# Kernel optimization log

Measured on AMD Instinct MI355X. Metric: run time of the kernel, lower is better.

## Reference

```python
import jax, jax.numpy as jnp
import numpy as np

B, D, H, W = 16, 128, 64, 64
K = 512  # num_embeddings


def setup_inputs() -> dict:
    key = jax.random.key(0)
    k1, k2 = jax.random.split(key)
    inputs = jax.random.normal(k1, (B, D, H, W), dtype=jnp.float32)
    embedding_weight = jax.random.normal(k2, (K, D), dtype=jnp.float32)
    return {"inputs": inputs, "embedding_weight": embedding_weight}


def reference(inputs, embedding_weight):
    # NCHW -> NHWC, flatten to [N, D]
    x = jnp.transpose(inputs, (0, 2, 3, 1))  # [B, H, W, D]
    flat = x.reshape(-1, x.shape[-1])        # [N, D]
    dists = (
        jnp.sum(flat ** 2, axis=1, keepdims=True)
        + jnp.sum(embedding_weight ** 2, axis=1)
        - 2.0 * flat @ embedding_weight.T
    )  # [N, K]
    idx = jnp.argmin(dists, axis=1)          # [N]
    # one-hot @ codebook == gather
    quantized = embedding_weight[idx].reshape(x.shape)  # [B, H, W, D]
    # straight-through estimator
    quantized = x + jax.lax.stop_gradient(quantized - x)
    return jnp.transpose(quantized, (0, 3, 1, 2))  # back to NCHW
```

## Files before the change

### kernel.cpp

```cpp
#include <hip/hip_runtime.h>


typedef _Float16 f16;
typedef _Float16 f16x4 __attribute__((ext_vector_type(4)));
typedef _Float16 f16x8 __attribute__((ext_vector_type(8)));
typedef float f32x16 __attribute__((ext_vector_type(16)));

#define ND 128
#define NK 512
#define NHW 4096
#define LO_SCALE 2048.0f
#define LO_INV (1.0f / 2048.0f)

#define WS_XHI 0
#define WS_XLO 16777216u
#define WS_EHI 33554432u
#define WS_ELO 33685504u
#define WS_ENS 33816576u
#define WS_NEED 33818624u

__global__ __launch_bounds__(256) void vq_prep(const float* __restrict__ x,
                                               const float* __restrict__ e,
                                               f16* __restrict__ xhi, f16* __restrict__ xlo,
                                               f16* __restrict__ ehi, f16* __restrict__ elo,
                                               float* __restrict__ ens) {
  const int tid = threadIdx.x;
  if (blockIdx.x < 1024) {
    __shared__ float sc[ND][65];
    const int tok0 = blockIdx.x * 64;
    const int b = blockIdx.x >> 6;
    const int hw0 = (blockIdx.x & 63) * 64;
    const float* xb = x + (size_t)b * ND * NHW + hw0;
    #pragma unroll
    for (int it = 0; it < 8; ++it) {
      const int f = tid + 256 * it;
      const int d = f >> 4, t4 = (f & 15) * 4;
      const float4 v = *(const float4*)(xb + (size_t)d * NHW + t4);
      sc[d][t4 + 0] = v.x; sc[d][t4 + 1] = v.y;
      sc[d][t4 + 2] = v.z; sc[d][t4 + 3] = v.w;
    }
    __syncthreads();
    const int oct = tid & 15, trow = tid >> 4;
    #pragma unroll
    for (int p = 0; p < 4; ++p) {
      const int t = p * 16 + trow;
      const int tok = tok0 + t;
      float v[8];
      #pragma unroll
      for (int j = 0; j < 8; ++j) v[j] = sc[oct * 8 + j][t];
      f16x8 h, l;
      #pragma unroll
      for (int j = 0; j < 8; ++j) {
        const f16 hv = (f16)v[j];
        h[j] = hv;
        l[j] = (f16)((v[j] - (float)hv) * LO_SCALE);
      }
      const size_t off = (size_t)(tok >> 5) * 4096 + oct * 256 + (tok & 31) * 8;
      *(f16x8*)(xhi + off) = h;
      *(f16x8*)(xlo + off) = l;
    }
  } else {
    const int k0 = ((int)blockIdx.x - 1024) * 16;
    const int r = tid >> 4, dq16 = tid & 15;
    const int k = k0 + r;
    float ssum = 0.0f;
    #pragma unroll
    for (int hh = 0; hh < 2; ++hh) {
      const int dq = dq16 + 16 * hh;
      const float4 v = *(const float4*)(e + (size_t)k * ND + 4 * dq);
      ssum += v.x * v.x + v.y * v.y + v.z * v.z + v.w * v.w;
      float va[4] = {v.x, v.y, v.z, v.w};
      f16x4 hv, lv;
      #pragma unroll
      for (int j = 0; j < 4; ++j) {
        const f16 h = (f16)va[j];
        hv[j] = h;
        lv[j] = (f16)((va[j] - (float)h) * LO_SCALE);
      }
      const int sl = (dq >> 1) ^ (k & 15);
      const size_t off = (size_t)k * ND + sl * 8 + (dq & 1) * 4;
      *(f16x4*)(ehi + off) = hv;
      *(f16x4*)(elo + off) = lv;
    }
    #pragma unroll
    for (int m = 1; m < 16; m <<= 1) ssum += __shfl_xor(ssum, m, 64);
    if (dq16 == 0) ens[k] = 0.5f * ssum;
  }
}

__global__ __launch_bounds__(256) void vq_score(const f16* __restrict__ xhi,
                                                const f16* __restrict__ xlo,
                                                const f16* __restrict__ ehi,
                                                const f16* __restrict__ elo,
                                                const float* __restrict__ ens,
                                                const float* __restrict__ e32,
                                                float* __restrict__ out) {
  __shared__ f16 eh_s[2][64 * 128];
  __shared__ f16 el_s[2][64 * 128];
  __shared__ float ens_s[NK];

  const int tid = threadIdx.x;
  const int w = tid >> 6;
  const int lane = tid & 63;
  const int l31 = lane & 31;
  const int half = lane >> 5;
  const int T0 = (int)blockIdx.x * 128;
  const int tok = T0 + w * 32 + l31;

  __builtin_amdgcn_global_load_lds(ehi + tid * 8,        &eh_s[0][tid * 8],        16, 0, 0);
  __builtin_amdgcn_global_load_lds(ehi + 2048 + tid * 8, &eh_s[0][2048 + tid * 8], 16, 0, 0);
  __builtin_amdgcn_global_load_lds(ehi + 4096 + tid * 8, &eh_s[0][4096 + tid * 8], 16, 0, 0);
  __builtin_amdgcn_global_load_lds(ehi + 6144 + tid * 8, &eh_s[0][6144 + tid * 8], 16, 0, 0);
  __builtin_amdgcn_global_load_lds(elo + tid * 8,        &el_s[0][tid * 8],        16, 0, 0);
  __builtin_amdgcn_global_load_lds(elo + 2048 + tid * 8, &el_s[0][2048 + tid * 8], 16, 0, 0);
  __builtin_amdgcn_global_load_lds(elo + 4096 + tid * 8, &el_s[0][4096 + tid * 8], 16, 0, 0);
  __builtin_amdgcn_global_load_lds(elo + 6144 + tid * 8, &el_s[0][6144 + tid * 8], 16, 0, 0);

  f16x8 Bh[8], Bl[8];
  {
    const size_t base = (size_t)(tok >> 5) * 4096 + (size_t)l31 * 8 + half * 256;
    #pragma unroll
    for (int ks = 0; ks < 8; ++ks) {
      Bh[ks] = *(const f16x8*)(xhi + base + ks * 512);
      Bl[ks] = *(const f16x8*)(xlo + base + ks * 512);
    }
  }
  ens_s[tid] = ens[tid];
  ens_s[tid + 256] = ens[tid + 256];
  __syncthreads();

  float bv = -3.0e38f;
  int bi = 0;
  int cur = 0;
  const int sbase = l31 & 15;

  for (int c = 0; c < 8; ++c) {
    if (c < 7) {
      const f16* gh = ehi + (c + 1) * 8192;
      const f16* gl = elo + (c + 1) * 8192;
      f16* dh = &eh_s[cur ^ 1][0];
      f16* dl = &el_s[cur ^ 1][0];
      __builtin_amdgcn_global_load_lds(gh + tid * 8,        dh + tid * 8,        16, 0, 0);
      __builtin_amdgcn_global_load_lds(gh + 2048 + tid * 8, dh + 2048 + tid * 8, 16, 0, 0);
      __builtin_amdgcn_global_load_lds(gh + 4096 + tid * 8, dh + 4096 + tid * 8, 16, 0, 0);
      __builtin_amdgcn_global_load_lds(gh + 6144 + tid * 8, dh + 6144 + tid * 8, 16, 0, 0);
      __builtin_amdgcn_global_load_lds(gl + tid * 8,        dl + tid * 8,        16, 0, 0);
      __builtin_amdgcn_global_load_lds(gl + 2048 + tid * 8, dl + 2048 + tid * 8, 16, 0, 0);
      __builtin_amdgcn_global_load_lds(gl + 4096 + tid * 8, dl + 4096 + tid * 8, 16, 0, 0);
      __builtin_amdgcn_global_load_lds(gl + 6144 + tid * 8, dl + 6144 + tid * 8, 16, 0, 0);
    }

    #pragma unroll
    for (int cg = 0; cg < 2; ++cg) {
      const int r = cg * 32 + l31;
      const f16* ah = &eh_s[cur][r * 128];
      const f16* al = &el_s[cur][r * 128];
      f32x16 a1 = {}, a2 = {};
      #pragma unroll
      for (int ks = 0; ks < 8; ++ks) {
        const int sl = ((2 * ks + half) ^ sbase) * 8;
        const f16x8 Ah = *(const f16x8*)(ah + sl);
        const f16x8 Al = *(const f16x8*)(al + sl);
        a2 = __builtin_amdgcn_mfma_f32_32x32x16_f16(Al, Bh[ks], a2, 0, 0, 0);
        a1 = __builtin_amdgcn_mfma_f32_32x32x16_f16(Ah, Bh[ks], a1, 0, 0, 0);
        a2 = __builtin_amdgcn_mfma_f32_32x32x16_f16(Ah, Bl[ks], a2, 0, 0, 0);
      }
      const int kb = c * 64 + cg * 32 + 4 * half;
      const float4 b0 = *(const float4*)&ens_s[kb + 0];
      const float4 b1 = *(const float4*)&ens_s[kb + 8];
      const float4 b2 = *(const float4*)&ens_s[kb + 16];
      const float4 b3 = *(const float4*)&ens_s[kb + 24];
      const float bias[16] = {b0.x, b0.y, b0.z, b0.w, b1.x, b1.y, b1.z, b1.w,
                              b2.x, b2.y, b2.z, b2.w, b3.x, b3.y, b3.z, b3.w};
      #pragma unroll
      for (int rr = 0; rr < 16; ++rr) {
        const float s = a1[rr] + a2[rr] * LO_INV - bias[rr];
        const int code = kb + (rr & 3) + 8 * (rr >> 2);
        if (s > bv) { bv = s; bi = code; }
      }
    }
    __syncthreads();
    cur ^= 1;
  }

  {
    const float ov = __shfl_xor(bv, 32, 64);
    const int oi = __shfl_xor(bi, 32, 64);
    if (ov > bv || (ov == bv && oi < bi)) { bv = ov; bi = oi; }
  }

  {
    const int bb = tok >> 12;
    const int hw = tok & 4095;
    const float* er = e32 + (size_t)bi * ND + half * 64;
    float* ob = out + (size_t)bb * ND * NHW + (size_t)(half * 64) * NHW + hw;
    #pragma unroll
    for (int j4 = 0; j4 < 16; ++j4) {
      const float4 ev = *(const float4*)(er + j4 * 4);
      ob[(size_t)(j4 * 4 + 0) * NHW] = ev.x;
      ob[(size_t)(j4 * 4 + 1) * NHW] = ev.y;
      ob[(size_t)(j4 * 4 + 2) * NHW] = ev.z;
      ob[(size_t)(j4 * 4 + 3) * NHW] = ev.w;
    }
  }
}

__global__ __launch_bounds__(128) void vq_enorm(const float* __restrict__ e,
                                                float* __restrict__ ensw) {
  const int k = blockIdx.x;
  const int d = threadIdx.x;
  const float v = e[k * ND + d];
  float s = v * v;
  #pragma unroll
  for (int off = 32; off > 0; off >>= 1) s += __shfl_down(s, off, 64);
  __shared__ float tmp[2];
  if ((d & 63) == 0) tmp[d >> 6] = s;
  __syncthreads();
  if (d == 0) ensw[k] = tmp[0] + tmp[1];
}

__global__ __launch_bounds__(256, 2) void vq_main_f32(const float* __restrict__ x,
                                                      const float* __restrict__ e,
                                                      const float* __restrict__ ensw,
                                                      float* __restrict__ out) {
  __shared__ float xs[ND][64];
  __shared__ float esh[ND][64];
  __shared__ float enh[NK];
  __shared__ float red_v[64][17];
  __shared__ int red_i[64][17];
  __shared__ int bidx[64];
  const int tid = threadIdx.x;
  const int b = blockIdx.x >> 6;
  const int hw0 = (blockIdx.x & 63) * 64;
  const float* xb = x + ((size_t)b * ND) * NHW;
  #pragma unroll
  for (int i = 0; i < 8; ++i) {
    const int f = tid + 256 * i;
    const int d = f >> 4, t4 = f & 15;
    const float4 v = *(const float4*)(xb + (size_t)d * NHW + hw0 + 4 * t4);
    *(float4*)&xs[d][4 * t4] = v;
  }
  #pragma unroll
  for (int i = 0; i < 2; ++i) enh[tid + 256 * i] = ensw[tid + 256 * i];
  const int t4 = tid & 15, m = tid >> 4;
  float bvv[4] = {-3.0e38f, -3.0e38f, -3.0e38f, -3.0e38f};
  int bii[4] = {0, 0, 0, 0};
  for (int kc = 0; kc < NK / 64; ++kc) {
    __syncthreads();
    #pragma unroll
    for (int i = 0; i < 8; ++i) {
      const int f = tid + 256 * i;
      const int kk = f & 63, dq = f >> 6;
      const float4 v = *(const float4*)(e + (size_t)(kc * 64 + kk) * ND + 4 * dq);
      esh[4 * dq + 0][kk] = v.x; esh[4 * dq + 1][kk] = v.y;
      esh[4 * dq + 2][kk] = v.z; esh[4 * dq + 3][kk] = v.w;
    }
    __syncthreads();
    float acc[4][4];
    #pragma unroll
    for (int a = 0; a < 4; ++a)
      #pragma unroll
      for (int cc = 0; cc < 4; ++cc) acc[a][cc] = 0.0f;
    #pragma unroll 8
    for (int d = 0; d < ND; ++d) {
      const float4 xv = *(const float4*)&xs[d][4 * t4];
      const float4 ev = *(const float4*)&esh[d][4 * m];
      const float xa[4] = {xv.x, xv.y, xv.z, xv.w};
      const float ea[4] = {ev.x, ev.y, ev.z, ev.w};
      #pragma unroll
      for (int a = 0; a < 4; ++a)
        #pragma unroll
        for (int cc = 0; cc < 4; ++cc) acc[a][cc] = fmaf(xa[a], ea[cc], acc[a][cc]);
    }
    const int kbase = kc * 64 + 4 * m;
    #pragma unroll
    for (int cc = 0; cc < 4; ++cc) {
      const float bias = 0.5f * enh[kbase + cc];
      const int kg = kbase + cc;
      #pragma unroll
      for (int a = 0; a < 4; ++a) {
        const float s = acc[a][cc] - bias;
        if (s > bvv[a] || (s == bvv[a] && kg < bii[a])) { bvv[a] = s; bii[a] = kg; }
      }
    }
  }
  #pragma unroll
  for (int a = 0; a < 4; ++a) { red_v[4 * t4 + a][m] = bvv[a]; red_i[4 * t4 + a][m] = bii[a]; }
  __syncthreads();
  if (tid < 64) {
    float v = red_v[tid][0]; int ix = red_i[tid][0];
    #pragma unroll
    for (int j = 1; j < 16; ++j) {
      const float vj = red_v[tid][j]; const int ij = red_i[tid][j];
      if (vj > v || (vj == v && ij < ix)) { v = vj; ix = ij; }
    }
    bidx[tid] = ix;
  }
  __syncthreads();
  const int t = tid & 63, dgg = tid >> 6;
  const float* er = e + (size_t)bidx[t] * ND;
  float* ob = out + ((size_t)b * ND) * NHW + hw0 + t;
  #pragma unroll
  for (int i = 0; i < 32; ++i) ob[(size_t)(dgg * 32 + i) * NHW] = er[dgg * 32 + i];
}

extern "C" void kernel_launch(void* const* d_in, const int* in_sizes, int n_in,
                              void* d_out, int out_size, void* d_ws, size_t ws_size,
                              hipStream_t stream) {
  const float* x = (const float*)d_in[0];
  const float* e = (const float*)d_in[1];
  float* out = (float*)d_out;
  char* ws = (char*)d_ws;

  if (ws_size >= WS_NEED) {
    f16* xhi = (f16*)(ws + WS_XHI);
    f16* xlo = (f16*)(ws + WS_XLO);
    f16* ehi = (f16*)(ws + WS_EHI);
    f16* elo = (f16*)(ws + WS_ELO);
    float* ens = (float*)(ws + WS_ENS);
    vq_prep<<<1056, 256, 0, stream>>>(x, e, xhi, xlo, ehi, elo, ens);
    vq_score<<<512, 256, 0, stream>>>(xhi, xlo, ehi, elo, ens, e, out);
  } else {
    float* ensw = (float*)d_ws;
    vq_enorm<<<NK, 128, 0, stream>>>(e, ensw);
    vq_main_f32<<<16 * 64, 256, 0, stream>>>(x, e, ensw, out);
  }
}
```

Before: 52.51 us.

## Fuse x hi/lo split into score kernel and single-buffer codebook LDS

Removes the separate x preprocessing pass that wrote f16 hi/lo copies of the whole input to workspace. The score kernel now reads fp32 x directly, coalesced along hw, and splits it into hi/lo fragments in registers. The codebook LDS staging drops from double to single buffering, with the next chunk loaded after a barrier, which halves LDS use but serialises load and compute. It also adds s_setprio around the MFMA loop. This saves a full write-and-reread of the input tensor in exchange for exposed codebook load latency.

```diff
diff --git a/kernel.cpp b/kernel.cpp
--- a/kernel.cpp
+++ b/kernel.cpp
@@ -12,91 +12,50 @@
 #define LO_SCALE 2048.0f
 #define LO_INV (1.0f / 2048.0f)
 
-#define WS_XHI 0
-#define WS_XLO 16777216u
-#define WS_EHI 33554432u
-#define WS_ELO 33685504u
-#define WS_ENS 33816576u
-#define WS_NEED 33818624u
-
-__global__ __launch_bounds__(256) void vq_prep(const float* __restrict__ x,
-                                               const float* __restrict__ e,
-                                               f16* __restrict__ xhi, f16* __restrict__ xlo,
-                                               f16* __restrict__ ehi, f16* __restrict__ elo,
-                                               float* __restrict__ ens) {
+#define WS_EHI 0
+#define WS_ELO 131072u
+#define WS_ENS 262144u
+#define WS_NEED 264192u
+
+__global__ __launch_bounds__(256) void vq_prep_e(const float* __restrict__ e,
+                                                 f16* __restrict__ ehi, f16* __restrict__ elo,
+                                                 float* __restrict__ ens) {
   const int tid = threadIdx.x;
-  if (blockIdx.x < 1024) {
-    __shared__ float sc[ND][65];
-    const int tok0 = blockIdx.x * 64;
-    const int b = blockIdx.x >> 6;
-    const int hw0 = (blockIdx.x & 63) * 64;
-    const float* xb = x + (size_t)b * ND * NHW + hw0;
-    #pragma unroll
-    for (int it = 0; it < 8; ++it) {
-      const int f = tid + 256 * it;
-      const int d = f >> 4, t4 = (f & 15) * 4;
-      const float4 v = *(const float4*)(xb + (size_t)d * NHW + t4);
-      sc[d][t4 + 0] = v.x; sc[d][t4 + 1] = v.y;
-      sc[d][t4 + 2] = v.z; sc[d][t4 + 3] = v.w;
-    }
-    __syncthreads();
-    const int oct = tid & 15, trow = tid >> 4;
-    #pragma unroll
-    for (int p = 0; p < 4; ++p) {
-      const int t = p * 16 + trow;
-      const int tok = tok0 + t;
-      float v[8];
-      #pragma unroll
-      for (int j = 0; j < 8; ++j) v[j] = sc[oct * 8 + j][t];
-      f16x8 h, l;
-      #pragma unroll
-      for (int j = 0; j < 8; ++j) {
-        const f16 hv = (f16)v[j];
-        h[j] = hv;
-        l[j] = (f16)((v[j] - (float)hv) * LO_SCALE);
-      }
-      const size_t off = (size_t)(tok >> 5) * 4096 + oct * 256 + (tok & 31) * 8;
-      *(f16x8*)(xhi + off) = h;
-      *(f16x8*)(xlo + off) = l;
-    }
-  } else {
-    const int k0 = ((int)blockIdx.x - 1024) * 16;
-    const int r = tid >> 4, dq16 = tid & 15;
-    const int k = k0 + r;
-    float ssum = 0.0f;
-    #pragma unroll
-    for (int hh = 0; hh < 2; ++hh) {
-      const int dq = dq16 + 16 * hh;
-      const float4 v = *(const float4*)(e + (size_t)k * ND + 4 * dq);
-      ssum += v.x * v.x + v.y * v.y + v.z * v.z + v.w * v.w;
-      float va[4] = {v.x, v.y, v.z, v.w};
-      f16x4 hv, lv;
-      #pragma unroll
-      for (int j = 0; j < 4; ++j) {
-        const f16 h = (f16)va[j];
-        hv[j] = h;
-        lv[j] = (f16)((va[j] - (float)h) * LO_SCALE);
-      }
-      const int sl = (dq >> 1) ^ (k & 15);
-      const size_t off = (size_t)k * ND + sl * 8 + (dq & 1) * 4;
-      *(f16x4*)(ehi + off) = hv;
-      *(f16x4*)(elo + off) = lv;
-    }
-    #pragma unroll
-    for (int m = 1; m < 16; m <<= 1) ssum += __shfl_xor(ssum, m, 64);
-    if (dq16 == 0) ens[k] = 0.5f * ssum;
-  }
-}
-
-__global__ __launch_bounds__(256) void vq_score(const f16* __restrict__ xhi,
-                                                const f16* __restrict__ xlo,
+  const int k0 = (int)blockIdx.x * 16;
+  const int r = tid >> 4, dq16 = tid & 15;
+  const int k = k0 + r;
+  float ssum = 0.0f;
+  #pragma unroll
+  for (int hh = 0; hh < 2; ++hh) {
+    const int dq = dq16 + 16 * hh;
+    const float4 v = *(const float4*)(e + (size_t)k * ND + 4 * dq);
+    ssum += v.x * v.x + v.y * v.y + v.z * v.z + v.w * v.w;
+    float va[4] = {v.x, v.y, v.z, v.w};
+    f16x4 hv, lv;
+    #pragma unroll
+    for (int j = 0; j < 4; ++j) {
+      const f16 h = (f16)va[j];
+      hv[j] = h;
+      lv[j] = (f16)((va[j] - (float)h) * LO_SCALE);
+    }
+    const int sl = (dq >> 1) ^ (k & 15);
+    const size_t off = (size_t)k * ND + sl * 8 + (dq & 1) * 4;
+    *(f16x4*)(ehi + off) = hv;
+    *(f16x4*)(elo + off) = lv;
+  }
+  #pragma unroll
+  for (int m = 1; m < 16; m <<= 1) ssum += __shfl_xor(ssum, m, 64);
+  if (dq16 == 0) ens[k] = 0.5f * ssum;
+}
+
+__global__ __launch_bounds__(256) void vq_score(const float* __restrict__ x,
                                                 const f16* __restrict__ ehi,
                                                 const f16* __restrict__ elo,
                                                 const float* __restrict__ ens,
                                                 const float* __restrict__ e32,
                                                 float* __restrict__ out) {
-  __shared__ f16 eh_s[2][64 * 128];
-  __shared__ f16 el_s[2][64 * 128];
+  __shared__ f16 eh_s[64 * 128];
+  __shared__ f16 el_s[64 * 128];
   __shared__ float ens_s[NK];
 
   const int tid = threadIdx.x;
@@ -106,23 +65,28 @@
   const int half = lane >> 5;
   const int T0 = (int)blockIdx.x * 128;
   const int tok = T0 + w * 32 + l31;
-
-  __builtin_amdgcn_global_load_lds(ehi + tid * 8,        &eh_s[0][tid * 8],        16, 0, 0);
-  __builtin_amdgcn_global_load_lds(ehi + 2048 + tid * 8, &eh_s[0][2048 + tid * 8], 16, 0, 0);
-  __builtin_amdgcn_global_load_lds(ehi + 4096 + tid * 8, &eh_s[0][4096 + tid * 8], 16, 0, 0);
-  __builtin_amdgcn_global_load_lds(ehi + 6144 + tid * 8, &eh_s[0][6144 + tid * 8], 16, 0, 0);
-  __builtin_amdgcn_global_load_lds(elo + tid * 8,        &el_s[0][tid * 8],        16, 0, 0);
-  __builtin_amdgcn_global_load_lds(elo + 2048 + tid * 8, &el_s[0][2048 + tid * 8], 16, 0, 0);
-  __builtin_amdgcn_global_load_lds(elo + 4096 + tid * 8, &el_s[0][4096 + tid * 8], 16, 0, 0);
-  __builtin_amdgcn_global_load_lds(elo + 6144 + tid * 8, &el_s[0][6144 + tid * 8], 16, 0, 0);
+  const int bb = tok >> 12;
+  const int hw = tok & 4095;
+
+  #pragma unroll
+  for (int p = 0; p < 4; ++p) {
+    __builtin_amdgcn_global_load_lds(ehi + p * 2048 + tid * 8, &eh_s[p * 2048 + tid * 8], 16, 0, 0);
+    __builtin_amdgcn_global_load_lds(elo + p * 2048 + tid * 8, &el_s[p * 2048 + tid * 8], 16, 0, 0);
+  }
 
   f16x8 Bh[8], Bl[8];
   {
-    const size_t base = (size_t)(tok >> 5) * 4096 + (size_t)l31 * 8 + half * 256;
+    const float* xb = x + (size_t)bb * ND * NHW + hw;
     #pragma unroll
     for (int ks = 0; ks < 8; ++ks) {
-      Bh[ks] = *(const f16x8*)(xhi + base + ks * 512);
-      Bl[ks] = *(const f16x8*)(xlo + base + ks * 512);
+      const int oct = 2 * ks + half;
+      #pragma unroll
+      for (int j = 0; j < 8; ++j) {
+        const float v = xb[(size_t)(oct * 8 + j) * NHW];
+        const f16 hv = (f16)v;
+        Bh[ks][j] = hv;
+        Bl[ks][j] = (f16)((v - (float)hv) * LO_SCALE);
+      }
     }
   }
   ens_s[tid] = ens[tid];
@@ -131,31 +95,16 @@
 
   float bv = -3.0e38f;
   int bi = 0;
-  int cur = 0;
   const int sbase = l31 & 15;
 
   for (int c = 0; c < 8; ++c) {
-    if (c < 7) {
-      const f16* gh = ehi + (c + 1) * 8192;
-      const f16* gl = elo + (c + 1) * 8192;
-      f16* dh = &eh_s[cur ^ 1][0];
-      f16* dl = &el_s[cur ^ 1][0];
-      __builtin_amdgcn_global_load_lds(gh + tid * 8,        dh + tid * 8,        16, 0, 0);
-      __builtin_amdgcn_global_load_lds(gh + 2048 + tid * 8, dh + 2048 + tid * 8, 16, 0, 0);
-      __builtin_amdgcn_global_load_lds(gh + 4096 + tid * 8, dh + 4096 + tid * 8, 16, 0, 0);
-      __builtin_amdgcn_global_load_lds(gh + 6144 + tid * 8, dh + 6144 + tid * 8, 16, 0, 0);
-      __builtin_amdgcn_global_load_lds(gl + tid * 8,        dl + tid * 8,        16, 0, 0);
-      __builtin_amdgcn_global_load_lds(gl + 2048 + tid * 8, dl + 2048 + tid * 8, 16, 0, 0);
-      __builtin_amdgcn_global_load_lds(gl + 4096 + tid * 8, dl + 4096 + tid * 8, 16, 0, 0);
-      __builtin_amdgcn_global_load_lds(gl + 6144 + tid * 8, dl + 6144 + tid * 8, 16, 0, 0);
-    }
-
     #pragma unroll
     for (int cg = 0; cg < 2; ++cg) {
       const int r = cg * 32 + l31;
-      const f16* ah = &eh_s[cur][r * 128];
-      const f16* al = &el_s[cur][r * 128];
+      const f16* ah = &eh_s[r * 128];
+      const f16* al = &el_s[r * 128];
       f32x16 a1 = {}, a2 = {};
+      __builtin_amdgcn_s_setprio(1);
       #pragma unroll
       for (int ks = 0; ks < 8; ++ks) {
         const int sl = ((2 * ks + half) ^ sbase) * 8;
@@ -165,6 +114,7 @@
         a1 = __builtin_amdgcn_mfma_f32_32x32x16_f16(Ah, Bh[ks], a1, 0, 0, 0);
         a2 = __builtin_amdgcn_mfma_f32_32x32x16_f16(Ah, Bl[ks], a2, 0, 0, 0);
       }
+      __builtin_amdgcn_s_setprio(0);
       const int kb = c * 64 + cg * 32 + 4 * half;
       const float4 b0 = *(const float4*)&ens_s[kb + 0];
       const float4 b1 = *(const float4*)&ens_s[kb + 8];
@@ -180,7 +130,16 @@
       }
     }
     __syncthreads();
-    cur ^= 1;
+    if (c < 7) {
+      const f16* gh = ehi + (c + 1) * 8192;
+      const f16* gl = elo + (c + 1) * 8192;
+      #pragma unroll
+      for (int p = 0; p < 4; ++p) {
+        __builtin_amdgcn_global_load_lds(gh + p * 2048 + tid * 8, &eh_s[p * 2048 + tid * 8], 16, 0, 0);
+        __builtin_amdgcn_global_load_lds(gl + p * 2048 + tid * 8, &el_s[p * 2048 + tid * 8], 16, 0, 0);
+      }
+      __syncthreads();
+    }
   }
 
   {
@@ -190,8 +149,6 @@
   }
 
   {
-    const int bb = tok >> 12;
-    const int hw = tok & 4095;
     const float* er = e32 + (size_t)bi * ND + half * 64;
     float* ob = out + (size_t)bb * ND * NHW + (size_t)(half * 64) * NHW + hw;
     #pragma unroll
@@ -313,13 +270,11 @@
   char* ws = (char*)d_ws;
 
   if (ws_size >= WS_NEED) {
-    f16* xhi = (f16*)(ws + WS_XHI);
-    f16* xlo = (f16*)(ws + WS_XLO);
     f16* ehi = (f16*)(ws + WS_EHI);
     f16* elo = (f16*)(ws + WS_ELO);
     float* ens = (float*)(ws + WS_ENS);
-    vq_prep<<<1056, 256, 0, stream>>>(x, e, xhi, xlo, ehi, elo, ens);
-    vq_score<<<512, 256, 0, stream>>>(xhi, xlo, ehi, elo, ens, e, out);
+    vq_prep_e<<<32, 256, 0, stream>>>(e, ehi, elo, ens);
+    vq_score<<<512, 256, 0, stream>>>(x, ehi, elo, ens, e, out);
   } else {
     float* ensw = (float*)d_ws;
     vq_enorm<<<NK, 128, 0, stream>>>(e, ensw);
```

Measured after the change: 45.45 us. 1.16x faster.
